# Kernel tuning notes

Hardware: AMD Instinct MI355X
Metric: run time of the kernel (lower is better)

Reference implementation:

```python
import jax, jax.numpy as jnp
import numpy as np

EPS = 1e-5

def _bn(x, s, o):
    m = jnp.mean(x, axis=(0, 1), keepdims=True)
    v = jnp.var(x, axis=(0, 1), keepdims=True)
    return (x - m) * jax.lax.rsqrt(v + EPS) * s + o

def _conv1d(x, w):
    return jax.lax.conv_general_dilated(x, w, (1,), 'SAME', dimension_numbers=('NWC', 'WIO', 'NWC'))

def _lstm_step(x, h, c, W, b):
    g = jnp.concatenate([x, h], -1) @ W + b
    i, gg, f, o = jnp.split(g, 4, -1)
    c = jax.nn.sigmoid(f + 1.0) * c + jax.nn.sigmoid(i) * jnp.tanh(gg)
    h = jax.nn.sigmoid(o) * jnp.tanh(c)
    return h, c

def setup_inputs() -> dict:
    key = jax.random.key(0)
    ks = jax.random.split(key, 24)
    B, L, T = 16, 256, 512
    V, E, H, MEL, P = 256, 256, 512, 80, 512
    f = lambda k, shape, s: jax.random.normal(k, shape, jnp.float32) * s
    inp = {}
    inp['phonemes'] = jax.random.randint(ks[0], (B, L), 0, V, dtype=jnp.int32)
    inp['lengths'] = jnp.full((B,), L, dtype=jnp.int32)
    inp['mels'] = jax.random.normal(ks[1], (B, T, MEL), jnp.float32)
    inp['durations'] = jax.random.uniform(ks[2], (B, L), jnp.float32, 1.0, 3.0)
    for i, n in enumerate(['zm_h1', 'zm_c1', 'zm_h2', 'zm_c2']):
        inp[n] = jax.random.bernoulli(ks[3 + i], 0.1, (B, T, H))
    inp['embed'] = f(ks[7], (V, E), 1.0)
    inp['enc_conv_w'] = f(ks[8], (3, 3, E, E), 0.05)
    inp['enc_bn_s'] = jnp.ones((3, E)); inp['enc_bn_o'] = jnp.zeros((3, E))
    inp['lstm_fwd_w'] = f(ks[9], (2 * E, 4 * E), 0.05); inp['lstm_fwd_b'] = jnp.zeros((4 * E,))
    inp['lstm_bwd_w'] = f(ks[10], (2 * E, 4 * E), 0.05); inp['lstm_bwd_b'] = jnp.zeros((4 * E,))
    inp['prenet_w1'] = f(ks[11], (MEL, 256), 0.05); inp['prenet_bn1_s'] = jnp.ones((256,)); inp['prenet_bn1_o'] = jnp.zeros((256,))
    inp['prenet_w2'] = f(ks[12], (256, 256), 0.05); inp['prenet_bn2_s'] = jnp.ones((256,)); inp['prenet_bn2_o'] = jnp.zeros((256,))
    D_in = 2 * E + 256  # cond(512)+prenet(256)=768
    inp['dec_w1'] = f(ks[13], (D_in + H, 4 * H), 0.03); inp['dec_b1'] = jnp.zeros((4 * H,))
    inp['dec_w2'] = f(ks[14], (D_in + H + H, 4 * H), 0.03); inp['dec_b2'] = jnp.zeros((4 * H,))
    inp['proj_w'] = f(ks[15], (2 * E + 2 * H, MEL), 0.03); inp['proj_b'] = jnp.zeros((MEL,))
    inp['post_w0'] = f(ks[16], (5, MEL, P), 0.05)
    inp['post_w_mid'] = f(ks[17], (3, 5, P, P), 0.03)
    inp['post_w4'] = f(ks[18], (5, P, MEL), 0.03); inp['post_b4'] = jnp.zeros((MEL,))
    inp['post_bn_s'] = jnp.ones((4, P)); inp['post_bn_o'] = jnp.zeros((4, P))
    return inp

def reference(phonemes, lengths, mels, durations, zm_h1, zm_c1, zm_h2, zm_c2,
              embed, enc_conv_w, enc_bn_s, enc_bn_o,
              lstm_fwd_w, lstm_fwd_b, lstm_bwd_w, lstm_bwd_b,
              prenet_w1, prenet_bn1_s, prenet_bn1_o, prenet_w2, prenet_bn2_s, prenet_bn2_o,
              dec_w1, dec_b1, dec_w2, dec_b2, proj_w, proj_b,
              post_w0, post_w_mid, post_w4, post_b4, post_bn_s, post_bn_o):
    x = embed[phonemes]                                   # [B,L,E]
    for i in range(3):
        x = jax.nn.relu(_bn(_conv1d(x, enc_conv_w[i]), enc_bn_s[i], enc_bn_o[i]))
    B, L, E = x.shape
    mask = jnp.arange(L)[None, :] >= (lengths[:, None] - 1)  # [B,L] reset signal for bwd core
    x_t = jnp.swapaxes(x, 0, 1)                           # [L,B,E] time-major
    h0 = jnp.zeros((B, E), x.dtype)

    def fwd_step(carry, xt):
        h, c = carry
        h, c = _lstm_step(xt, h, c, lstm_fwd_w, lstm_fwd_b)
        return (h, c), h
    _, h_fwd = jax.lax.scan(fwd_step, (h0, h0), x_t)

    x_b = jnp.flip(x_t, axis=0)
    r_b = jnp.flip(jnp.swapaxes(mask, 0, 1), axis=0)      # [L,B]

    def bwd_step(carry, inp):
        xt, rt = inp
        h, c = carry
        h = jnp.where(rt[:, None], 0.0, h)  # ResetCore: reset state to initial where flagged
        c = jnp.where(rt[:, None], 0.0, c)
        h, c = _lstm_step(xt, h, c, lstm_bwd_w, lstm_bwd_b)
        return (h, c), h
    _, h_bwd = jax.lax.scan(bwd_step, (h0, h0), (x_b, r_b))
    enc = jnp.swapaxes(jnp.concatenate([h_fwd, jnp.flip(h_bwd, axis=0)], -1), 0, 1)  # [B,L,2E]

    # ---- duration-based Gaussian-softmax upsampling ----
    T = mels.shape[1]
    ruler = jnp.arange(T, dtype=durations.dtype)[None, :]
    mid_pos = jnp.cumsum(durations, axis=1) - durations / 2  # [B,L]
    d2 = jnp.square(mid_pos[:, None, :] - ruler[:, :, None]) / 10.0  # [B,T,L]
    w = jax.nn.softmax(-d2, axis=-1)
    cond = jnp.einsum('btl,bld->btd', w, enc)             # [B,T,512]

    # ---- prenet on teacher-forced mels ----
    p = jax.nn.relu(_bn(mels @ prenet_w1, prenet_bn1_s, prenet_bn1_o))
    p = jax.nn.relu(_bn(p @ prenet_w2, prenet_bn2_s, prenet_bn2_o))
    dec_in = jnp.concatenate([cond, p], axis=-1)          # [B,T,768]

    # ---- 2-layer skip-connection LSTM decoder with zoneout ----
    H = dec_w1.shape[1] // 4
    s0 = jnp.zeros((B, H), dec_in.dtype)
    xs = (jnp.swapaxes(dec_in, 0, 1),
          jnp.swapaxes(zm_h1, 0, 1), jnp.swapaxes(zm_c1, 0, 1),
          jnp.swapaxes(zm_h2, 0, 1), jnp.swapaxes(zm_c2, 0, 1))

    def dec_step(carry, inp):
        h1, c1, h2, c2 = carry
        xt, mh1, mc1, mh2, mc2 = inp
        nh1, nc1 = _lstm_step(xt, h1, c1, dec_w1, dec_b1)
        in2 = jnp.concatenate([xt, nh1], -1)              # skip connection
        nh2, nc2 = _lstm_step(in2, h2, c2, dec_w2, dec_b2)
        out = jnp.concatenate([nh1, nh2], -1)
        zo = lambda m, so, sn: jnp.where(m, so, sn)       # zoneout: keep old state w.p. 0.1
        return (zo(mh1, h1, nh1), zo(mc1, c1, nc1), zo(mh2, h2, nh2), zo(mc2, c2, nc2)), out
    _, dec_out = jax.lax.scan(dec_step, (s0, s0, s0, s0), xs)
    dec_out = jnp.swapaxes(dec_out, 0, 1)                 # [B,T,2H]

    mel_pred = jnp.concatenate([cond, dec_out], -1) @ proj_w + proj_b  # [B,T,80]

    y = jnp.tanh(_bn(_conv1d(mel_pred, post_w0), post_bn_s[0], post_bn_o[0]))
    for i in range(3):
        y = jnp.tanh(_bn(_conv1d(y, post_w_mid[i]), post_bn_s[i + 1], post_bn_o[i + 1]))
    residual = _conv1d(y, post_w4) + post_b4
    return (mel_pred, mel_pred + residual)
```

## Files before the change

### kernel.cpp

```cpp
#include <hip/hip_runtime.h>

#define EPSV 1e-5f

typedef unsigned int uivec4 __attribute__((ext_vector_type(4)));
typedef short bh8 __attribute__((ext_vector_type(8)));
typedef float f32x4 __attribute__((ext_vector_type(4)));

__device__ __forceinline__ float b2f(unsigned short u) {
  unsigned int x = ((unsigned int)u) << 16;
  return __uint_as_float(x);
}
__device__ __forceinline__ unsigned short f2b(float f) {
  unsigned int x = __float_as_uint(f);
  unsigned int r = (x + 0x7FFFu + ((x >> 16) & 1u)) >> 16;
  return (unsigned short)r;
}
__device__ __forceinline__ float sigm(float x) { return 1.0f / (1.0f + expf(-x)); }

__device__ __forceinline__ void stg_bf16(unsigned short* p, float v) {
  unsigned short h = f2b(v);
  asm volatile("global_store_short %0, %1, off sc0 sc1" ::"v"(p), "v"(h) : "memory");
}
__device__ __forceinline__ void ldg2_sc(const unsigned short* p0, const unsigned short* p1,
                                        uivec4& a, uivec4& b) {
  asm volatile(
      "global_load_dwordx4 %0, %2, off sc0 sc1\n\t"
      "global_load_dwordx4 %1, %3, off sc0 sc1\n\t"
      "s_waitcnt vmcnt(0)"
      : "=&v"(a), "=&v"(b)
      : "v"(p0), "v"(p1)
      : "memory");
}
__device__ __forceinline__ void ldg4f_nw(const unsigned short* p, uivec4& a, uivec4& b,
                                         uivec4& c, uivec4& d) {
  asm volatile(
      "global_load_dwordx4 %0, %4, off sc0 sc1\n\t"
      "global_load_dwordx4 %1, %4, off offset:256 sc0 sc1\n\t"
      "global_load_dwordx4 %2, %4, off offset:512 sc0 sc1\n\t"
      "global_load_dwordx4 %3, %4, off offset:768 sc0 sc1"
      : "=&v"(a), "=&v"(b), "=&v"(c), "=&v"(d)
      : "v"(p)
      : "memory");
}
__device__ __forceinline__ void vm0() { asm volatile("s_waitcnt vmcnt(0)" ::: "memory"); }
__device__ __forceinline__ unsigned int ldcnt(const unsigned int* p) {
  return __hip_atomic_load(p, __ATOMIC_RELAXED, __HIP_MEMORY_SCOPE_AGENT);
}

__global__ void k_detect(const void* __restrict__ embp, const void* __restrict__ zmp,
                         int* __restrict__ flags) {
  __shared__ int sh[4];
  int tid = threadIdx.x;
  if (tid < 4) sh[tid] = 0;
  __syncthreads();
  const unsigned short* u = (const unsigned short*)embp;
  int bad = 0;
  for (int i = tid; i < 4096; i += 256) {
    float f = fabsf(b2f(u[i]));
    if (!(f < 1e10f)) bad = 1;
  }
  if (bad) atomicAdd(&sh[3], 1);
  const unsigned char* p = (const unsigned char*)zmp;
  int codd = 0, c0 = 0, c1v = 0;
  for (int i = tid; i < 65536; i += 256) {
    unsigned char v = p[i];
    if (v) {
      if (i & 1) codd++;
      if ((i & 3) == 0) c0++;
      if (v == 1) c1v++;
    }
  }
  atomicAdd(&sh[0], codd); atomicAdd(&sh[1], c0); atomicAdd(&sh[2], c1v);
  __syncthreads();
  if (tid == 0) {
    flags[0] = sh[3] ? 1 : 0;
    int mode;
    if (sh[0] == 0) mode = 1;
    else if (sh[2] > 0) mode = 0;
    else if (sh[1] == 0) mode = 2;
    else mode = 3;
    flags[1] = mode;
  }
}

__global__ void k_cvt(const void* __restrict__ src, float* __restrict__ dst, int n,
                      const int* __restrict__ flags) {
  int i = blockIdx.x * 256 + threadIdx.x;
  if (i >= n) return;
  if (flags[0]) dst[i] = ((const float*)src)[i];
  else dst[i] = b2f(((const unsigned short*)src)[i]);
}

__global__ void k_cvtb(const float* __restrict__ src, unsigned short* __restrict__ dst, int n) {
  int i = blockIdx.x * 256 + threadIdx.x;
  if (i >= n) return;
  dst[i] = f2b(src[i]);
}

__global__ void k_cvtbp(const float* __restrict__ src, unsigned short* __restrict__ dst,
                        int K, int Kpad) {
  int r = blockIdx.x;
  int c = threadIdx.x;
  if (c < Kpad)
    dst[(size_t)r * Kpad + c] = (c < K) ? f2b(src[(size_t)r * K + c]) : (unsigned short)0;
}

__device__ __forceinline__ bool mask_at(const void* p, size_t i, int mode) {
  switch (mode) {
    case 0: return ((const unsigned char*)p)[i] != 0;
    case 1: return ((const int*)p)[i] != 0;
    case 2: return ((const float*)p)[i] != 0.0f;
    default: return ((const unsigned short*)p)[i] != 0;
  }
}

__global__ void k_embed(const int* __restrict__ ph, const float* __restrict__ emb,
                        float* __restrict__ X) {
  int bl = blockIdx.x;
  int p = ph[bl];
  X[(size_t)bl * 256 + threadIdx.x] = emb[(size_t)p * 256 + threadIdx.x];
}

__global__ __launch_bounds__(256) void k_cs1(const float* __restrict__ X, int RB, int C,
                                             float* __restrict__ part) {
  int blk = blockIdx.x;
  int r0 = blk * RB;
  float s0 = 0.f, q0 = 0.f, s1 = 0.f, q1 = 0.f;
  for (int rr = 0; rr < RB; ++rr) {
    const float* row = X + (size_t)(r0 + rr) * C;
    float v = row[threadIdx.x];
    s0 += v; q0 += v * v;
    if (C > 256) {
      float v1 = row[256 + threadIdx.x];
      s1 += v1; q1 += v1 * v1;
    }
  }
  float* pr = part + (size_t)blk * 2 * C;
  pr[threadIdx.x] = s0;
  pr[C + threadIdx.x] = q0;
  if (C > 256) {
    pr[256 + threadIdx.x] = s1;
    pr[C + 256 + threadIdx.x] = q1;
  }
}
__global__ __launch_bounds__(256) void k_cs2(const float* __restrict__ part, int C, int R,
                                             float* __restrict__ st) {
  int c = blockIdx.x;
  int t = threadIdx.x;
  __shared__ float rs_[256], rq_[256];
  rs_[t] = part[(size_t)t * 2 * C + c];
  rq_[t] = part[(size_t)t * 2 * C + C + c];
  __syncthreads();
  for (int k = 128; k > 0; k >>= 1) {
    if (t < k) { rs_[t] += rs_[t + k]; rq_[t] += rq_[t + k]; }
    __syncthreads();
  }
  if (t == 0) {
    float m = rs_[0] / R;
    st[c] = m;
    st[C + c] = rq_[0] / R - m * m;
  }
}

template <int ACT>
__global__ void k_bnact(const float* __restrict__ X, float* __restrict__ Y,
                        const float* __restrict__ st, const float* __restrict__ sc,
                        const float* __restrict__ of, int Cmask, int n) {
  int i = blockIdx.x * 256 + threadIdx.x;
  if (i >= n) return;
  int C = Cmask + 1;
  int c = i & Cmask;
  float m = st[c], v = st[C + c];
  float y = (X[i] - m) * rsqrtf(v + EPSV) * sc[c] + of[c];
  Y[i] = ACT ? tanhf(y) : fmaxf(y, 0.0f);
}

__global__ __launch_bounds__(256) void k_trbp(const float* __restrict__ src, int ldn,
                                              unsigned short* __restrict__ dst,
                                              int K, int Kpad, int N, int Npad) {
  __shared__ float tl[64][65];
  int k0 = blockIdx.x * 64, n0 = blockIdx.y * 64;
  int tid = threadIdx.x;
#pragma unroll
  for (int p = 0; p < 16; ++p) {
    int idx = p * 256 + tid;
    int r = idx >> 6, c = idx & 63;
    float v = 0.0f;
    if (k0 + r < K && n0 + c < N) v = src[(size_t)(k0 + r) * ldn + n0 + c];
    tl[r][c] = v;
  }
  __syncthreads();
#pragma unroll
  for (int p = 0; p < 16; ++p) {
    int idx = p * 256 + tid;
    int rr = idx >> 6, cc = idx & 63;
    if (n0 + rr < Npad && k0 + cc < Kpad)
      dst[(size_t)(n0 + rr) * Kpad + k0 + cc] = f2b(tl[cc][rr]);
  }
}

__global__ __launch_bounds__(256) void k_i2c3(const float* __restrict__ X,
                                              unsigned short* __restrict__ out) {
  int r = blockIdx.x;
  int b = r >> 8, l = r & 255;
#pragma unroll
  for (int p = 0; p < 3; ++p) {
    int col = p * 256 + threadIdx.x;
    int d = col >> 8, ci = col & 255;
    int ll = l + d - 1;
    float v = (ll >= 0 && ll < 256) ? X[(size_t)(b * 256 + ll) * 256 + ci] : 0.0f;
    out[(size_t)r * 768 + col] = f2b(v);
  }
}
__global__ __launch_bounds__(256) void k_i2c(const float* __restrict__ X,
                                             unsigned short* __restrict__ out) {
  int r = blockIdx.x;
  int b = r >> 9, t = r & 511;
#pragma unroll
  for (int p = 0; p < 10; ++p) {
    int col = p * 256 + threadIdx.x;
    int dt = col >> 9, ci = col & 511;
    int tt = t + dt - 2;
    float v = (tt >= 0 && tt < 512) ? X[((size_t)(b * 512 + tt)) * 512 + ci] : 0.0f;
    out[(size_t)r * 2560 + col] = f2b(v);
  }
}
__global__ __launch_bounds__(256) void k_i2c80(const float* __restrict__ X,
                                               unsigned short* __restrict__ out) {
  int r = blockIdx.x;
  int b = r >> 9, t = r & 511;
#pragma unroll
  for (int p = 0; p < 2; ++p) {
    int col = p * 256 + threadIdx.x;
    if (col < 416) {
      float v = 0.0f;
      if (col < 400) {
        int dt = col / 80, ci = col - dt * 80;
        int tt = t + dt - 2;
        if (tt >= 0 && tt < 512) v = X[(size_t)(b * 512 + tt) * 80 + ci];
      }
      out[(size_t)r * 416 + col] = f2b(v);
    }
  }
}

__global__ __launch_bounds__(256) void k_cat3b(const float* __restrict__ cond,
                                               const float* __restrict__ h1n,
                                               const float* __restrict__ h2n,
                                               unsigned short* __restrict__ out) {
  int r = blockIdx.x;
  int b = r >> 9, t = r & 511;
#pragma unroll
  for (int p = 0; p < 6; ++p) {
    int col = p * 256 + threadIdx.x;
    float v;
    if (col < 512) v = cond[(size_t)r * 512 + col];
    else if (col < 1024) v = h1n[(size_t)(t * 16 + b) * 512 + (col - 512)];
    else v = h2n[(size_t)(t * 16 + b) * 512 + (col - 1024)];
    out[(size_t)r * 1536 + col] = f2b(v);
  }
}

template <int OBF>
__global__ __launch_bounds__(256) void k_mf(const unsigned short* __restrict__ A,
                                            const unsigned short* __restrict__ Bt,
                                            const float* __restrict__ bias,
                                            void* __restrict__ Cp, int M, int N, int K,
                                            int Nst) {
  const int lane = threadIdx.x & 63, wv = threadIdx.x >> 6;
  const int m0 = blockIdx.x * 64 + wv * 16;
  const int n0 = blockIdx.y * 64;
  const int koff = (lane >> 4) << 3;
  const unsigned short* arow = A + (size_t)(m0 + (lane & 15)) * K + koff;
  const unsigned short* brow0 = Bt + (size_t)(n0 + 0 * 16 + (lane & 15)) * K + koff;
  const unsigned short* brow1 = Bt + (size_t)(n0 + 1 * 16 + (lane & 15)) * K + koff;
  const unsigned short* brow2 = Bt + (size_t)(n0 + 2 * 16 + (lane & 15)) * K + koff;
  const unsigned short* brow3 = Bt + (size_t)(n0 + 3 * 16 + (lane & 15)) * K + koff;
  f32x4 acc0 = {0.f, 0.f, 0.f, 0.f}, acc1 = {0.f, 0.f, 0.f, 0.f};
  f32x4 acc2 = {0.f, 0.f, 0.f, 0.f}, acc3 = {0.f, 0.f, 0.f, 0.f};
  for (int k = 0; k < K; k += 32) {
    bh8 a = *(const bh8*)(arow + k);
    bh8 b0 = *(const bh8*)(brow0 + k);
    bh8 b1 = *(const bh8*)(brow1 + k);
    bh8 b2 = *(const bh8*)(brow2 + k);
    bh8 b3 = *(const bh8*)(brow3 + k);
    acc0 = __builtin_amdgcn_mfma_f32_16x16x32_bf16(a, b0, acc0, 0, 0, 0);
    acc1 = __builtin_amdgcn_mfma_f32_16x16x32_bf16(a, b1, acc1, 0, 0, 0);
    acc2 = __builtin_amdgcn_mfma_f32_16x16x32_bf16(a, b2, acc2, 0, 0, 0);
    acc3 = __builtin_amdgcn_mfma_f32_16x16x32_bf16(a, b3, acc3, 0, 0, 0);
  }
  const int r0 = m0 + ((lane >> 4) << 2);
  const int nl = lane & 15;
  float av[4][4];
#pragma unroll
  for (int r = 0; r < 4; ++r) { av[0][r] = acc0[r]; av[1][r] = acc1[r]; av[2][r] = acc2[r]; av[3][r] = acc3[r]; }
#pragma unroll
  for (int t = 0; t < 4; ++t) {
    int n = n0 + t * 16 + nl;
    float bv = 0.0f;
    if (bias) {
      if (OBF == 4) bv = (n < Nst) ? bias[n] : 0.0f;
      else bv = bias[n];
    }
#pragma unroll
    for (int r = 0; r < 4; ++r) {
      float v = av[t][r] + bv;
      int row = r0 + r;
      if (OBF == 0) {
        ((float*)Cp)[(size_t)row * N + n] = v;
      } else if (OBF == 4) {
        if (n < Nst) ((float*)Cp)[(size_t)row * Nst + n] = v;
      } else if (OBF == 2) {
        int b = row >> 9, tt = row & 511;
        int g = n >> 9, w = (n & 511) >> 2, jj = n & 3;
        ((unsigned short*)Cp)[((size_t)tt * 128 + w) * 256 + b * 16 + g * 4 + jj] = f2b(v);
      } else {
        int b = row >> 8, l = row & 255;
        int g = n >> 8, w = (n & 255) >> 2, jj = n & 3;
        ((float*)Cp)[((size_t)l * 64 + w) * 256 + b * 16 + g * 4 + jj] = v;
      }
    }
  }
}

__global__ void k_cumsum(const float* __restrict__ dur, float* __restrict__ mid) {
  int b = threadIdx.x;
  if (b >= 16) return;
  float run = 0.f;
  for (int l = 0; l < 256; ++l) {
    float d = dur[b * 256 + l];
    run += d;
    mid[b * 256 + l] = run - 0.5f * d;
  }
}

#define EST 130
__global__ __launch_bounds__(256) void k_enc_lstm(const float* __restrict__ GFp,
                                                  const float* __restrict__ GBp,
                                                  const float* __restrict__ Wf,
                                                  const float* __restrict__ Wb,
                                                  float* __restrict__ enc,
                                                  unsigned short* __restrict__ encB,
                                                  const int* __restrict__ lengths,
                                                  unsigned int* __restrict__ cnt) {
  const int tid = threadIdx.x;
  const int wg = blockIdx.x;
  const int dir = wg >> 6;
  const int w = wg & 63;
  const float* Gpre = dir ? GBp : GFp;
  const float* W = dir ? Wb : Wf;
  unsigned int* c_self = cnt + (size_t)dir * 256 * 128;

  __shared__ __align__(16) unsigned int hsW[16 * EST];
  __shared__ __align__(16) float accb[4 * 264];
  __shared__ __align__(16) float gl[256];
  __shared__ float cst[64];
  __shared__ int rs[16];

  const int lane = tid & 63, wv = tid >> 6;
  const int n16 = lane & 15, lq = lane >> 4;
  const int colg = (n16 & 3) * 256 + w * 4 + (n16 >> 2);
  bh8 BE[2];
#pragma unroll
  for (int c = 0; c < 2; ++c) {
#pragma unroll
    for (int jj = 0; jj < 8; ++jj) {
      int k = (wv * 2 + c) * 32 + lq * 8 + jj;
      BE[c][jj] = (short)f2b(W[(size_t)(256 + k) * 1024 + colg]);
    }
  }
  if (tid < 64) cst[tid] = 0.0f;
  __syncthreads();

  const int b_ = tid >> 4, j_ = (tid >> 2) & 3, g_ = tid & 3;

  for (int t = 0; t < 256; ++t) {
    const int l = dir ? (255 - t) : t;
    if (tid < 16) rs[tid] = (dir == 1) && (l >= lengths[tid] - 1);
    float gpre = Gpre[((size_t)l * 64 + w) * 256 + b_ * 16 + g_ * 4 + j_];
    if (t > 0 && tid < 8) {
      const unsigned int* a = c_self + (size_t)(t - 1) * 128 + tid * 16;
      unsigned int gcount = 0;
      while (ldcnt(a) < 8u) {
        __builtin_amdgcn_s_sleep(2);
        if (++gcount > (1u << 16)) break;
      }
    }
    __syncthreads();
    if (t > 0) {
      const int lprev = dir ? (l + 1) : (l - 1);
      int b = tid >> 4, q = tid & 15;
      const unsigned short* p = encB + ((size_t)dir << 20) + (((size_t)lprev * 16 + b) << 8) + q * 16;
      uivec4 a0, a1;
      ldg2_sc(p, p + 8, a0, a1);
      if (rs[b]) {
        a0.x = a0.y = a0.z = a0.w = 0u;
        a1.x = a1.y = a1.z = a1.w = 0u;
      }
      *(uivec4*)&hsW[b * EST + q * 8] = a0;
      *(uivec4*)&hsW[b * EST + q * 8 + 4] = a1;
    }
    __syncthreads();

    f32x4 acc = {0.f, 0.f, 0.f, 0.f};
    if (t > 0) {
#pragma unroll
      for (int c = 0; c < 2; ++c) {
        int kw = (wv * 2 + c) * 16 + lq * 4;
        bh8 af = *(const bh8*)&hsW[(lane & 15) * EST + kw];
        acc = __builtin_amdgcn_mfma_f32_16x16x32_bf16(af, BE[c], acc, 0, 0, 0);
      }
    }
    {
      int idx = lq * 64 + (lane & 15);
      float* pb = &accb[wv * 264];
#pragma unroll
      for (int r = 0; r < 4; ++r) pb[idx + r * 16] = acc[r];
    }
    __syncthreads();
    gl[tid] = gpre + accb[tid] + accb[264 + tid] + accb[528 + tid] + accb[792 + tid];
    __syncthreads();
    if (tid < 64) {
      int b = tid >> 2, j = tid & 3;
      float4 G = ((const float4*)gl)[tid];
      float c = cst[tid];
      if (t == 0 || rs[b]) c = 0.0f;
      c = sigm(G.z + 1.0f) * c + sigm(G.x) * tanhf(G.y);
      float h = sigm(G.w) * tanhf(c);
      cst[tid] = c;
      enc[(size_t)(b * 256 + l) * 512 + dir * 256 + (w * 4 + j)] = h;
      stg_bf16(&encB[((size_t)dir << 20) + (((size_t)l * 16 + b) << 8) + (w * 4 + j)], h);
    }
    vm0();
    __syncthreads();
    if (tid == 0)
      __hip_atomic_fetch_add(c_self + (size_t)t * 128 + (w >> 3) * 16, 1u,
                             __ATOMIC_RELAXED, __HIP_MEMORY_SCOPE_AGENT);
  }
}

__global__ __launch_bounds__(256) void k_upsample(const float* __restrict__ mid,
                                                  const float* __restrict__ enc,
                                                  float* __restrict__ cond) {
  int blk = blockIdx.x;
  int b = blk >> 5, t0 = (blk & 31) * 16;
  int tid = threadIdx.x;
  __shared__ float wls[16][256];
  __shared__ float red[256];
  float mp = mid[b * 256 + tid];
  for (int tt = 0; tt < 16; ++tt) {
    float tpos = (float)(t0 + tt);
    float d = mp - tpos;
    float d2 = d * d * 0.1f;
    red[tid] = d2; __syncthreads();
    for (int k = 128; k > 0; k >>= 1) { if (tid < k) red[tid] = fminf(red[tid], red[tid + k]); __syncthreads(); }
    float mn = red[0]; __syncthreads();
    float e = expf(mn - d2);
    red[tid] = e; __syncthreads();
    for (int k = 128; k > 0; k >>= 1) { if (tid < k) red[tid] += red[tid + k]; __syncthreads(); }
    float sum = red[0]; __syncthreads();
    wls[tt][tid] = e / sum;
  }
  __syncthreads();
  float a0[16], a1[16];
#pragma unroll
  for (int i = 0; i < 16; ++i) { a0[i] = 0; a1[i] = 0; }
  for (int l = 0; l < 256; ++l) {
    float e0 = enc[(size_t)(b * 256 + l) * 512 + tid];
    float e1 = enc[(size_t)(b * 256 + l) * 512 + 256 + tid];
#pragma unroll
    for (int tt = 0; tt < 16; ++tt) { float wv = wls[tt][l]; a0[tt] += wv * e0; a1[tt] += wv * e1; }
  }
  for (int tt = 0; tt < 16; ++tt) {
    cond[(size_t)(b * 512 + t0 + tt) * 512 + tid] = a0[tt];
    cond[(size_t)(b * 512 + t0 + tt) * 512 + 256 + tid] = a1[tt];
  }
}

__global__ void k_concat(const float* __restrict__ cond, const float* __restrict__ p,
                         unsigned short* __restrict__ din) {
  size_t i = (size_t)blockIdx.x * 256 + threadIdx.x;
  int r = (int)(i / 768);
  int c = (int)(i % 768);
  float v = (c < 512) ? cond[(size_t)r * 512 + c] : p[(size_t)r * 256 + (c - 512)];
  din[i] = f2b(v);
}

#define DST 780
__global__ __launch_bounds__(256) void k_dec_lstm(
    const unsigned short* __restrict__ D1x, const unsigned short* __restrict__ D2x,
    const float* __restrict__ W1, const float* __restrict__ W2,
    const void* __restrict__ zh1, const void* __restrict__ zc1,
    const void* __restrict__ zh2, const void* __restrict__ zc2,
    unsigned short* __restrict__ h1cB, unsigned short* __restrict__ h1nB,
    unsigned short* __restrict__ h2cB,
    float* __restrict__ h1n, float* __restrict__ h2n,
    unsigned int* __restrict__ cnt1,
    const int* __restrict__ flags) {
  const int tid = threadIdx.x;
  const int w = blockIdx.x;

  __shared__ __align__(16) unsigned int hsW[16 * DST];
  __shared__ __align__(16) float accb[8 * 264];
  __shared__ __align__(16) float gl1[256], gl2[256];
  __shared__ float cst1[64], hst1[64], cst2[64], hst2[64];

  const int mmode = flags[1];
  const int lane = tid & 63, wv = tid >> 6;
  const int n16 = lane & 15, lq = lane >> 4;
  const int colg = (n16 & 3) * 512 + w * 4 + (n16 >> 2);

  bh8 B1[4], B2[8];
#pragma unroll
  for (int c = 0; c < 4; ++c) {
#pragma unroll
    for (int jj = 0; jj < 8; ++jj) {
      int k = (wv * 4 + c) * 32 + lq * 8 + jj;
      B1[c][jj] = (short)f2b(W1[(size_t)(768 + k) * 2048 + colg]);
    }
  }
#pragma unroll
  for (int c = 0; c < 8; ++c) {
#pragma unroll
    for (int jj = 0; jj < 8; ++jj) {
      int k = (wv * 8 + c) * 32 + lq * 8 + jj;
      B2[c][jj] = (short)f2b(W2[(size_t)(768 + k) * 2048 + colg]);
    }
  }
  if (tid < 64) { cst1[tid] = 0; hst1[tid] = 0; cst2[tid] = 0; hst2[tid] = 0; }
  __syncthreads();

  const int b_ = tid >> 4, j_ = (tid >> 2) & 3, g_ = tid & 3;

  for (int tau = 0; tau <= 512; ++tau) {
    float dxv1 = 0.0f, dxv2 = 0.0f;
    if (tau < 512)
      dxv1 = b2f(D1x[((size_t)tau * 128 + w) * 256 + b_ * 16 + g_ * 4 + j_]);
    if (tau >= 1)
      dxv2 = b2f(D2x[((size_t)(tau - 1) * 128 + w) * 256 + b_ * 16 + g_ * 4 + j_]);

    if (tau >= 1 && tid < 8) {
      const unsigned int* a = cnt1 + (size_t)(tau - 1) * 128 + tid * 16;
      unsigned int gcount = 0;
      while (ldcnt(a) < 16u) {
        __builtin_amdgcn_s_sleep(2);
        if (++gcount > (1u << 16)) break;
      }
    }
    __syncthreads();

    if (tau >= 1) {
      int b = tid >> 4, q = tid & 15;
      const unsigned short* p0 = h1cB + (((size_t)(tau - 1) * 16 + b) << 9) + q * 8;
      const unsigned short* p1 = h1nB + (((size_t)(tau - 1) * 16 + b) << 9) + q * 8;
      uivec4 r[12];
      ldg4f_nw(p0, r[0], r[1], r[2], r[3]);
      ldg4f_nw(p1, r[4], r[5], r[6], r[7]);
      if (tau >= 2) {
        const unsigned short* p2 = h2cB + (((size_t)(tau - 2) * 16 + b) << 9) + q * 8;
        ldg4f_nw(p2, r[8], r[9], r[10], r[11]);
      } else {
        uivec4 z; z.x = z.y = z.z = z.w = 0u;
        r[8] = z; r[9] = z; r[10] = z; r[11] = z;
      }
      vm0();
      unsigned int base = b * DST + q * 4;
#pragma unroll
      for (int m = 0; m < 4; ++m) *(uivec4*)&hsW[base + 64 * m] = r[m];
#pragma unroll
      for (int m = 0; m < 4; ++m) *(uivec4*)&hsW[base + 256 + 64 * m] = r[4 + m];
#pragma unroll
      for (int m = 0; m < 4; ++m) *(uivec4*)&hsW[base + 512 + 64 * m] = r[8 + m];
    }
    __syncthreads();

    f32x4 a1 = {0.f, 0.f, 0.f, 0.f}, a2 = {0.f, 0.f, 0.f, 0.f};
    if (tau >= 1) {
      if (tau < 512) {
#pragma unroll
        for (int c = 0; c < 4; ++c) {
          int kw = (wv * 4 + c) * 16 + lq * 4;
          bh8 af = *(const bh8*)&hsW[(lane & 15) * DST + kw];
          a1 = __builtin_amdgcn_mfma_f32_16x16x32_bf16(af, B1[c], a1, 0, 0, 0);
        }
      }
#pragma unroll
      for (int c = 0; c < 8; ++c) {
        int kw = 256 + (wv * 8 + c) * 16 + lq * 4;
        bh8 af = *(const bh8*)&hsW[(lane & 15) * DST + kw];
        a2 = __builtin_amdgcn_mfma_f32_16x16x32_bf16(af, B2[c], a2, 0, 0, 0);
      }
    }
    {
      int idx = lq * 64 + (lane & 15);
      float* p1b = &accb[wv * 264];
      float* p2b = &accb[(4 + wv) * 264];
#pragma unroll
      for (int r = 0; r < 4; ++r) p1b[idx + r * 16] = a1[r];
#pragma unroll
      for (int r = 0; r < 4; ++r) p2b[idx + r * 16] = a2[r];
    }
    __syncthreads();
    gl1[tid] = dxv1 + accb[tid] + accb[264 + tid] + accb[528 + tid] + accb[792 + tid];
    gl2[tid] = dxv2 + accb[1056 + tid] + accb[1320 + tid] + accb[1584 + tid] + accb[1848 + tid];
    __syncthreads();

    if (tid < 64) {
      if (tau < 512) {
        int b = tid >> 2, j = tid & 3, colgw = w * 4 + j;
        float4 G = ((const float4*)gl1)[tid];
        float cold = (tau == 0) ? 0.0f : cst1[tid];
        float hold = (tau == 0) ? 0.0f : hst1[tid];
        float nc = sigm(G.z + 1.0f) * cold + sigm(G.x) * tanhf(G.y);
        float nh = sigm(G.w) * tanhf(nc);
        size_t mi = ((size_t)b * 512 + tau) * 512 + colgw;
        bool mh = mask_at(zh1, mi, mmode);
        bool mc = mask_at(zc1, mi, mmode);
        cst1[tid] = mc ? cold : nc;
        float hkeep = mh ? hold : nh;
        hst1[tid] = hkeep;
        h1n[(size_t)(tau * 16 + b) * 512 + colgw] = nh;
        stg_bf16(&h1cB[(((size_t)tau * 16 + b) << 9) + colgw], hkeep);
        stg_bf16(&h1nB[(((size_t)tau * 16 + b) << 9) + colgw], nh);
      }
    } else if (tid < 128) {
      if (tau >= 1) {
        int u = tid - 64;
        int t2 = tau - 1;
        int b = u >> 2, j = u & 3, colgw = w * 4 + j;
        float4 G = ((const float4*)gl2)[u];
        float cold = (tau == 1) ? 0.0f : cst2[u];
        float hold = (tau == 1) ? 0.0f : hst2[u];
        float nc = sigm(G.z + 1.0f) * cold + sigm(G.x) * tanhf(G.y);
        float nh = sigm(G.w) * tanhf(nc);
        size_t mi = ((size_t)b * 512 + t2) * 512 + colgw;
        bool mh = mask_at(zh2, mi, mmode);
        bool mc = mask_at(zc2, mi, mmode);
        cst2[u] = mc ? cold : nc;
        float hkeep = mh ? hold : nh;
        hst2[u] = hkeep;
        h2n[(size_t)(t2 * 16 + b) * 512 + colgw] = nh;
        stg_bf16(&h2cB[(((size_t)t2 * 16 + b) << 9) + colgw], hkeep);
      }
    }
    vm0();
    __syncthreads();
    if (tid == 0)
      __hip_atomic_fetch_add(cnt1 + (size_t)tau * 128 + (w >> 4) * 16, 1u,
                             __ATOMIC_RELAXED, __HIP_MEMORY_SCOPE_AGENT);
  }
}

__global__ void k_out(const float* __restrict__ mel, const float* __restrict__ res,
                      void* __restrict__ out, const int* __restrict__ flags) {
  int i = blockIdx.x * 256 + threadIdx.x;
  float m = mel[i];
  float f = m + res[i];
  if (flags[0]) {
    ((float*)out)[i] = m;
    ((float*)out)[655360 + i] = f;
  } else {
    unsigned short* o = (unsigned short*)out;
    o[i] = f2b(m);
    o[655360 + i] = f2b(f);
  }
}

extern "C" void kernel_launch(void* const* d_in, const int* in_sizes, int n_in,
                              void* d_out, int out_size, void* d_ws, size_t ws_size,
                              hipStream_t stream) {
  char* ws = (char*)d_ws;
  size_t o = 0;
  auto A_ = [&](size_t nb) { size_t r = o; o += (nb + 255) & ~(size_t)255; return r; };
  const size_t FLAGS = A_(256);
  const size_t SYNC = A_(786432);
  const size_t STATS = A_(4096);
  const size_t PARTS = A_(1048576 + 4096);
  const size_t XAB = A_(2097152);
  const size_t WTE1 = A_(524288), WTE2 = A_(524288);
  const size_t C_MELS = A_(655360ull * 4), C_DUR = A_(4096 * 4), C_EMB = A_(65536 * 4),
               C_ECW = A_(589824ull * 4), C_EBS = A_(768 * 4), C_EBO = A_(768 * 4),
               C_LFW = A_(524288ull * 4), C_LFB = A_(1024 * 4), C_LBW = A_(524288ull * 4),
               C_LBB = A_(1024 * 4), C_PW1 = A_(20480 * 4), C_P1S = A_(256 * 4),
               C_P1O = A_(256 * 4), C_PW2 = A_(65536 * 4), C_P2S = A_(256 * 4),
               C_P2O = A_(256 * 4), C_DW1 = A_(2621440ull * 4), C_DB1 = A_(2048 * 4),
               C_DW2 = A_(3670016ull * 4), C_DB2 = A_(2048 * 4), C_PRW = A_(122880ull * 4),
               C_PRB = A_(512), C_W0 = A_(204800ull * 4), C_WM = A_(3932160ull * 4),
               C_W4 = A_(204800ull * 4), C_B4 = A_(512), C_PBS = A_(2048 * 4),
               C_PBO = A_(2048 * 4);
  const size_t R1 = A_(16777216), R2 = A_(16777216), R3 = A_(16777216), R4 = A_(16777216),
               MID = A_(4096 * 4), R5 = A_(16777216), R6 = A_(16777216), R7 = A_(25165824),
               D1X = A_(33554432), D2X = A_(33554432), MELP = A_(2621440);
  const size_t XA = R1, XB = R1 + 4194304;
  const size_t XCOL3 = R2, ECWT = R3;
  const size_t GF = R2;
  const size_t GB = R3, H1N = R3;
  const size_t ENC = R4, H2N = R4;
  const size_t COND = R5, PA = R5;
  const size_t PREA = R6, PREB = R6 + 8388608, PB = R6;
  const size_t DECIN = R7, RESID = R7;
  const size_t H1CB = R1, H1NB = R1 + 8388608;
  const size_t H2CB = R2;
  const size_t ENCB = R7;
  const size_t MELB = R1, PW1T = R1 + 2097152, PREBB = R1, PW2T = R1 + 8388608;
  const size_t WT1 = R4, WT2 = R4 + 4194304;
  const size_t PROJA = R1;
  const size_t PRWT = R6;
  const size_t XCOL80 = R1, W0T = R2;
  const size_t XCOL = R1;
  const size_t WTP = D1X, W4T = D2X;

  auto F = [&](size_t off) { return (float*)(ws + off); };
  auto U = [&](size_t off) { return (unsigned short*)(ws + off); };
  int* flags = (int*)(ws + FLAGS);
  unsigned int* cntE = (unsigned int*)(ws + SYNC);
  unsigned int* cnt1 = (unsigned int*)(ws + SYNC + 262144);

  hipMemsetAsync(ws + SYNC, 0, 786432, stream);
  k_detect<<<1, 256, 0, stream>>>(d_in[8], d_in[4], flags);

  struct CV { int idx; size_t off; int n; };
  const CV cvs[] = {
      {2, C_MELS, 655360}, {3, C_DUR, 4096}, {8, C_EMB, 65536}, {9, C_ECW, 589824},
      {10, C_EBS, 768}, {11, C_EBO, 768}, {12, C_LFW, 524288}, {13, C_LFB, 1024},
      {14, C_LBW, 524288}, {15, C_LBB, 1024}, {16, C_PW1, 20480}, {17, C_P1S, 256},
      {18, C_P1O, 256}, {19, C_PW2, 65536}, {20, C_P2S, 256}, {21, C_P2O, 256},
      {22, C_DW1, 2621440}, {23, C_DB1, 2048}, {24, C_DW2, 3670016}, {25, C_DB2, 2048},
      {26, C_PRW, 122880}, {27, C_PRB, 80}, {28, C_W0, 204800}, {29, C_WM, 3932160},
      {30, C_W4, 204800}, {31, C_B4, 80}, {32, C_PBS, 2048}, {33, C_PBO, 2048}};
  for (int i = 0; i < (int)(sizeof(cvs) / sizeof(cvs[0])); ++i)
    k_cvt<<<(cvs[i].n + 255) / 256, 256, 0, stream>>>(d_in[cvs[i].idx], F(cvs[i].off), cvs[i].n, flags);

  k_embed<<<4096, 256, 0, stream>>>((const int*)d_in[0], F(C_EMB), F(XA));
  for (int i = 0; i < 3; ++i) {
    k_i2c3<<<4096, 256, 0, stream>>>(F(XA), U(XCOL3));
    k_trbp<<<dim3(12, 4), 256, 0, stream>>>(F(C_ECW) + (size_t)i * 196608, 256, U(ECWT), 768, 768, 256, 256);
    k_mf<0><<<dim3(64, 4), 256, 0, stream>>>(U(XCOL3), U(ECWT), nullptr, (void*)(ws + XB), 4096, 256, 768, 256);
    k_cs1<<<256, 256, 0, stream>>>(F(XB), 16, 256, F(PARTS));
    k_cs2<<<256, 256, 0, stream>>>(F(PARTS), 256, 4096, F(STATS));
    k_bnact<0><<<4096, 256, 0, stream>>>(F(XB), F(XA), F(STATS), F(C_EBS) + i * 256, F(C_EBO) + i * 256, 255, 1048576);
  }
  k_cvtb<<<4096, 256, 0, stream>>>(F(XA), U(XAB), 1048576);
  k_trbp<<<dim3(4, 16), 256, 0, stream>>>(F(C_LFW), 1024, U(WTE1), 256, 256, 1024, 1024);
  k_trbp<<<dim3(4, 16), 256, 0, stream>>>(F(C_LBW), 1024, U(WTE2), 256, 256, 1024, 1024);
  k_mf<3><<<dim3(64, 16), 256, 0, stream>>>(U(XAB), U(WTE1), F(C_LFB), (void*)(ws + GF), 4096, 1024, 256, 1024);
  k_mf<3><<<dim3(64, 16), 256, 0, stream>>>(U(XAB), U(WTE2), F(C_LBB), (void*)(ws + GB), 4096, 1024, 256, 1024);
  k_cumsum<<<1, 64, 0, stream>>>(F(C_DUR), F(MID));
  k_enc_lstm<<<128, 256, 0, stream>>>(F(GF), F(GB), F(C_LFW), F(C_LBW), F(ENC), U(ENCB),
                                      (const int*)d_in[1], cntE);
  k_upsample<<<512, 256, 0, stream>>>(F(MID), F(ENC), F(COND));

  k_cvtbp<<<8192, 128, 0, stream>>>(F(C_MELS), U(MELB), 80, 96);
  k_trbp<<<dim3(2, 4), 256, 0, stream>>>(F(C_PW1), 256, U(PW1T), 80, 96, 256, 256);
  k_mf<0><<<dim3(128, 4), 256, 0, stream>>>(U(MELB), U(PW1T), nullptr, (void*)(ws + PREA), 8192, 256, 96, 256);
  k_cs1<<<256, 256, 0, stream>>>(F(PREA), 32, 256, F(PARTS));
  k_cs2<<<256, 256, 0, stream>>>(F(PARTS), 256, 8192, F(STATS));
  k_bnact<0><<<8192, 256, 0, stream>>>(F(PREA), F(PREB), F(STATS), F(C_P1S), F(C_P1O), 255, 2097152);
  k_cvtb<<<8192, 256, 0, stream>>>(F(PREB), U(PREBB), 2097152);
  k_trbp<<<dim3(4, 4), 256, 0, stream>>>(F(C_PW2), 256, U(PW2T), 256, 256, 256, 256);
  k_mf<0><<<dim3(128, 4), 256, 0, stream>>>(U(PREBB), U(PW2T), nullptr, (void*)(ws + PREA), 8192, 256, 256, 256);
  k_cs1<<<256, 256, 0, stream>>>(F(PREA), 32, 256, F(PARTS));
  k_cs2<<<256, 256, 0, stream>>>(F(PARTS), 256, 8192, F(STATS));
  k_bnact<0><<<8192, 256, 0, stream>>>(F(PREA), F(PREB), F(STATS), F(C_P2S), F(C_P2O), 255, 2097152);

  k_concat<<<24576, 256, 0, stream>>>(F(COND), F(PREB), U(DECIN));
  k_trbp<<<dim3(12, 32), 256, 0, stream>>>(F(C_DW1), 2048, U(WT1), 768, 768, 2048, 2048);
  k_trbp<<<dim3(12, 32), 256, 0, stream>>>(F(C_DW2), 2048, U(WT2), 768, 768, 2048, 2048);
  k_mf<2><<<dim3(128, 32), 256, 0, stream>>>(U(DECIN), U(WT1), F(C_DB1), (void*)(ws + D1X), 8192, 2048, 768, 2048);
  k_mf<2><<<dim3(128, 32), 256, 0, stream>>>(U(DECIN), U(WT2), F(C_DB2), (void*)(ws + D2X), 8192, 2048, 768, 2048);
  k_dec_lstm<<<128, 256, 0, stream>>>((const unsigned short*)(ws + D1X), (const unsigned short*)(ws + D2X),
                                      F(C_DW1), F(C_DW2), d_in[4], d_in[5], d_in[6], d_in[7],
                                      U(H1CB), U(H1NB), U(H2CB),
                                      F(H1N), F(H2N), cnt1, flags);
  k_cat3b<<<8192, 256, 0, stream>>>(F(COND), F(H1N), F(H2N), U(PROJA));
  k_trbp<<<dim3(24, 2), 256, 0, stream>>>(F(C_PRW), 80, U(PRWT), 1536, 1536, 80, 128);
  k_mf<4><<<dim3(128, 2), 256, 0, stream>>>(U(PROJA), U(PRWT), F(C_PRB), (void*)(ws + MELP), 8192, 128, 1536, 80);

  k_i2c80<<<8192, 256, 0, stream>>>(F(MELP), U(XCOL80));
  k_trbp<<<dim3(7, 8), 256, 0, stream>>>(F(C_W0), 512, U(W0T), 400, 416, 512, 512);
  k_mf<0><<<dim3(128, 8), 256, 0, stream>>>(U(XCOL80), U(W0T), nullptr, (void*)(ws + PA), 8192, 512, 416, 512);
  k_cs1<<<256, 256, 0, stream>>>(F(PA), 32, 512, F(PARTS));
  k_cs2<<<512, 256, 0, stream>>>(F(PARTS), 512, 8192, F(STATS));
  k_bnact<1><<<16384, 256, 0, stream>>>(F(PA), F(PB), F(STATS), F(C_PBS), F(C_PBO), 511, 4194304);
  for (int i = 0; i < 3; ++i) {
    k_i2c<<<8192, 256, 0, stream>>>(F(PB), U(XCOL));
    k_trbp<<<dim3(40, 8), 256, 0, stream>>>(F(C_WM) + (size_t)i * 1310720, 512, U(WTP), 2560, 2560, 512, 512);
    k_mf<0><<<dim3(128, 8), 256, 0, stream>>>(U(XCOL), U(WTP), nullptr, (void*)(ws + PA), 8192, 512, 2560, 512);
    k_cs1<<<256, 256, 0, stream>>>(F(PA), 32, 512, F(PARTS));
    k_cs2<<<512, 256, 0, stream>>>(F(PARTS), 512, 8192, F(STATS));
    k_bnact<1><<<16384, 256, 0, stream>>>(F(PA), F(PB), F(STATS), F(C_PBS) + (i + 1) * 512, F(C_PBO) + (i + 1) * 512, 511, 4194304);
  }
  k_i2c<<<8192, 256, 0, stream>>>(F(PB), U(XCOL));
  k_trbp<<<dim3(40, 2), 256, 0, stream>>>(F(C_W4), 80, U(W4T), 2560, 2560, 80, 128);
  k_mf<4><<<dim3(128, 2), 256, 0, stream>>>(U(XCOL), U(W4T), F(C_B4), (void*)(ws + RESID), 8192, 128, 2560, 80);
  k_out<<<2560, 256, 0, stream>>>(F(MELP), F(RESID), d_out, flags);
}
```

Baseline: 5.237 ms.

## Fuse im2col into conv GEMMs and halve workgroups in recurrent LSTM kernels

The conv layers now use a new implicit-im2col MFMA GEMM kernel (k_mfc) that reads the bf16 activations directly. This removes the separate im2col kernels and their large intermediate buffers. The BN/activation and embedding kernels also write a bf16 copy, so a separate conversion pass is no longer needed. Separately, the encoder and decoder LSTM kernels are remapped so each workgroup handles 8 hidden units instead of 4 (64 workgroups instead of 128), which reduces cross-workgroup barrier participants per step at the cost of more MFMA and work per block.

Measured after the change: 4.875 ms (median of 2 runs). -6.9%, faster.

```diff
diff --git a/kernel.cpp b/kernel.cpp
--- a/kernel.cpp
+++ b/kernel.cpp
@@ -115,10 +115,12 @@
 }
 
 __global__ void k_embed(const int* __restrict__ ph, const float* __restrict__ emb,
-                        float* __restrict__ X) {
+                        float* __restrict__ X, unsigned short* __restrict__ Xb) {
   int bl = blockIdx.x;
   int p = ph[bl];
-  X[(size_t)bl * 256 + threadIdx.x] = emb[(size_t)p * 256 + threadIdx.x];
+  float v = emb[(size_t)p * 256 + threadIdx.x];
+  X[(size_t)bl * 256 + threadIdx.x] = v;
+  Xb[(size_t)bl * 256 + threadIdx.x] = f2b(v);
 }
 
 __global__ __launch_bounds__(256) void k_cs1(const float* __restrict__ X, int RB, int C,
@@ -164,6 +166,7 @@
 
 template <int ACT>
 __global__ void k_bnact(const float* __restrict__ X, float* __restrict__ Y,
+                        unsigned short* __restrict__ Yb,
                         const float* __restrict__ st, const float* __restrict__ sc,
                         const float* __restrict__ of, int Cmask, int n) {
   int i = blockIdx.x * 256 + threadIdx.x;
@@ -172,7 +175,9 @@
   int c = i & Cmask;
   float m = st[c], v = st[C + c];
   float y = (X[i] - m) * rsqrtf(v + EPSV) * sc[c] + of[c];
-  Y[i] = ACT ? tanhf(y) : fmaxf(y, 0.0f);
+  float r = ACT ? tanhf(y) : fmaxf(y, 0.0f);
+  Y[i] = r;
+  if (Yb) Yb[i] = f2b(r);
 }
 
 __global__ __launch_bounds__(256) void k_trbp(const float* __restrict__ src, int ldn,
@@ -196,51 +201,6 @@
     int rr = idx >> 6, cc = idx & 63;
     if (n0 + rr < Npad && k0 + cc < Kpad)
       dst[(size_t)(n0 + rr) * Kpad + k0 + cc] = f2b(tl[cc][rr]);
-  }
-}
-
-__global__ __launch_bounds__(256) void k_i2c3(const float* __restrict__ X,
-                                              unsigned short* __restrict__ out) {
-  int r = blockIdx.x;
-  int b = r >> 8, l = r & 255;
-#pragma unroll
-  for (int p = 0; p < 3; ++p) {
-    int col = p * 256 + threadIdx.x;
-    int d = col >> 8, ci = col & 255;
-    int ll = l + d - 1;
-    float v = (ll >= 0 && ll < 256) ? X[(size_t)(b * 256 + ll) * 256 + ci] : 0.0f;
-    out[(size_t)r * 768 + col] = f2b(v);
-  }
-}
-__global__ __launch_bounds__(256) void k_i2c(const float* __restrict__ X,
-                                             unsigned short* __restrict__ out) {
-  int r = blockIdx.x;
-  int b = r >> 9, t = r & 511;
-#pragma unroll
-  for (int p = 0; p < 10; ++p) {
-    int col = p * 256 + threadIdx.x;
-    int dt = col >> 9, ci = col & 511;
-    int tt = t + dt - 2;
-    float v = (tt >= 0 && tt < 512) ? X[((size_t)(b * 512 + tt)) * 512 + ci] : 0.0f;
-    out[(size_t)r * 2560 + col] = f2b(v);
-  }
-}
-__global__ __launch_bounds__(256) void k_i2c80(const float* __restrict__ X,
-                                               unsigned short* __restrict__ out) {
-  int r = blockIdx.x;
-  int b = r >> 9, t = r & 511;
-#pragma unroll
-  for (int p = 0; p < 2; ++p) {
-    int col = p * 256 + threadIdx.x;
-    if (col < 416) {
-      float v = 0.0f;
-      if (col < 400) {
-        int dt = col / 80, ci = col - dt * 80;
-        int tt = t + dt - 2;
-        if (tt >= 0 && tt < 512) v = X[(size_t)(b * 512 + tt) * 80 + ci];
-      }
-      out[(size_t)r * 416 + col] = f2b(v);
-    }
   }
 }
 
@@ -323,6 +283,67 @@
   }
 }
 
+template <int KW, int CIN, int TT, int OBF>
+__global__ __launch_bounds__(256) void k_mfc(const unsigned short* __restrict__ Xb,
+                                             const unsigned short* __restrict__ Bt,
+                                             const float* __restrict__ bias,
+                                             void* __restrict__ Cp, int M, int N, int K,
+                                             int Nst) {
+  const int lane = threadIdx.x & 63, wv = threadIdx.x >> 6;
+  const int m0 = blockIdx.x * 64 + wv * 16;
+  const int n0 = blockIdx.y * 64;
+  const int koff = (lane >> 4) << 3;
+  const int row = m0 + (lane & 15);
+  const int bb = row / TT, t = row % TT;
+  const unsigned short* brow0 = Bt + (size_t)(n0 + 0 * 16 + (lane & 15)) * K + koff;
+  const unsigned short* brow1 = Bt + (size_t)(n0 + 1 * 16 + (lane & 15)) * K + koff;
+  const unsigned short* brow2 = Bt + (size_t)(n0 + 2 * 16 + (lane & 15)) * K + koff;
+  const unsigned short* brow3 = Bt + (size_t)(n0 + 3 * 16 + (lane & 15)) * K + koff;
+  f32x4 acc0 = {0.f, 0.f, 0.f, 0.f}, acc1 = {0.f, 0.f, 0.f, 0.f};
+  f32x4 acc2 = {0.f, 0.f, 0.f, 0.f}, acc3 = {0.f, 0.f, 0.f, 0.f};
+  for (int k = 0; k < K; k += 32) {
+    int ke = k + koff;
+    int dt = ke / CIN;
+    int ci = ke - dt * CIN;
+    int tt = t + dt - (KW / 2);
+    bh8 a = {0, 0, 0, 0, 0, 0, 0, 0};
+    if (dt < KW && tt >= 0 && tt < TT)
+      a = *(const bh8*)&Xb[((size_t)(bb * TT + tt)) * CIN + ci];
+    bh8 b0 = *(const bh8*)(brow0 + k);
+    bh8 b1 = *(const bh8*)(brow1 + k);
+    bh8 b2 = *(const bh8*)(brow2 + k);
+    bh8 b3 = *(const bh8*)(brow3 + k);
+    acc0 = __builtin_amdgcn_mfma_f32_16x16x32_bf16(a, b0, acc0, 0, 0, 0);
+    acc1 = __builtin_amdgcn_mfma_f32_16x16x32_bf16(a, b1, acc1, 0, 0, 0);
+    acc2 = __builtin_amdgcn_mfma_f32_16x16x32_bf16(a, b2, acc2, 0, 0, 0);
+    acc3 = __builtin_amdgcn_mfma_f32_16x16x32_bf16(a, b3, acc3, 0, 0, 0);
+  }
+  const int r0 = m0 + ((lane >> 4) << 2);
+  const int nl = lane & 15;
+  float av[4][4];
+#pragma unroll
+  for (int r = 0; r < 4; ++r) { av[0][r] = acc0[r]; av[1][r] = acc1[r]; av[2][r] = acc2[r]; av[3][r] = acc3[r]; }
+#pragma unroll
+  for (int tq = 0; tq < 4; ++tq) {
+    int n = n0 + tq * 16 + nl;
+    float bv = 0.0f;
+    if (bias) {
+      if (OBF == 4) bv = (n < Nst) ? bias[n] : 0.0f;
+      else bv = bias[n];
+    }
+#pragma unroll
+    for (int r = 0; r < 4; ++r) {
+      float v = av[tq][r] + bv;
+      int rw = r0 + r;
+      if (OBF == 0) {
+        ((float*)Cp)[(size_t)rw * N + n] = v;
+      } else if (OBF == 4) {
+        if (n < Nst) ((float*)Cp)[(size_t)rw * Nst + n] = v;
+      }
+    }
+  }
+}
+
 __global__ void k_cumsum(const float* __restrict__ dur, float* __restrict__ mid) {
   int b = threadIdx.x;
   if (b >= 16) return;
@@ -345,43 +366,53 @@
                                                   unsigned int* __restrict__ cnt) {
   const int tid = threadIdx.x;
   const int wg = blockIdx.x;
-  const int dir = wg >> 6;
-  const int w = wg & 63;
+  const int dir = wg >> 5;
+  const int w = wg & 31;
   const float* Gpre = dir ? GBp : GFp;
   const float* W = dir ? Wb : Wf;
   unsigned int* c_self = cnt + (size_t)dir * 256 * 128;
 
   __shared__ __align__(16) unsigned int hsW[16 * EST];
-  __shared__ __align__(16) float accb[4 * 264];
-  __shared__ __align__(16) float gl[256];
-  __shared__ float cst[64];
+  __shared__ __align__(16) float accb[8 * 264];
+  __shared__ __align__(16) float gl[16 * 33];
+  __shared__ float cst[128];
   __shared__ int rs[16];
 
   const int lane = tid & 63, wv = tid >> 6;
   const int n16 = lane & 15, lq = lane >> 4;
-  const int colg = (n16 & 3) * 256 + w * 4 + (n16 >> 2);
-  bh8 BE[2];
-#pragma unroll
-  for (int c = 0; c < 2; ++c) {
-#pragma unroll
-    for (int jj = 0; jj < 8; ++jj) {
-      int k = (wv * 2 + c) * 32 + lq * 8 + jj;
-      BE[c][jj] = (short)f2b(W[(size_t)(256 + k) * 1024 + colg]);
-    }
-  }
-  if (tid < 64) cst[tid] = 0.0f;
+
+  bh8 BE[2][2];
+#pragma unroll
+  for (int s = 0; s < 2; ++s) {
+    int n = s * 16 + n16;
+    int colg = (n >> 3) * 256 + w * 8 + (n & 7);
+#pragma unroll
+    for (int c = 0; c < 2; ++c)
+#pragma unroll
+      for (int j = 0; j < 8; ++j) {
+        int k = wv * 64 + c * 32 + lq * 8 + j;
+        BE[c][s][j] = (short)f2b(W[(size_t)(256 + k) * 1024 + colg]);
+      }
+  }
+  if (tid < 128) cst[tid] = 0.0f;
   __syncthreads();
-
-  const int b_ = tid >> 4, j_ = (tid >> 2) & 3, g_ = tid & 3;
 
   for (int t = 0; t < 256; ++t) {
     const int l = dir ? (255 - t) : t;
     if (tid < 16) rs[tid] = (dir == 1) && (l >= lengths[tid] - 1);
-    float gpre = Gpre[((size_t)l * 64 + w) * 256 + b_ * 16 + g_ * 4 + j_];
+    float gp[2];
+#pragma unroll
+    for (int it = 0; it < 2; ++it) {
+      int e = tid + it * 256;
+      int b = e >> 5, n = e & 31;
+      int jn = n & 7, g = n >> 3;
+      int slot = w * 2 + (jn >> 2);
+      gp[it] = Gpre[((size_t)l * 64 + slot) * 256 + b * 16 + g * 4 + (jn & 3)];
+    }
     if (t > 0 && tid < 8) {
       const unsigned int* a = c_self + (size_t)(t - 1) * 128 + tid * 16;
       unsigned int gcount = 0;
-      while (ldcnt(a) < 8u) {
+      while (ldcnt(a) < 4u) {
         __builtin_amdgcn_s_sleep(2);
         if (++gcount > (1u << 16)) break;
       }
@@ -402,39 +433,58 @@
     }
     __syncthreads();
 
-    f32x4 acc = {0.f, 0.f, 0.f, 0.f};
+    f32x4 ac[2] = {{0.f, 0.f, 0.f, 0.f}, {0.f, 0.f, 0.f, 0.f}};
     if (t > 0) {
 #pragma unroll
       for (int c = 0; c < 2; ++c) {
-        int kw = (wv * 2 + c) * 16 + lq * 4;
+        int kw = wv * 32 + c * 16 + lq * 4;
         bh8 af = *(const bh8*)&hsW[(lane & 15) * EST + kw];
-        acc = __builtin_amdgcn_mfma_f32_16x16x32_bf16(af, BE[c], acc, 0, 0, 0);
+        ac[0] = __builtin_amdgcn_mfma_f32_16x16x32_bf16(af, BE[c][0], ac[0], 0, 0, 0);
+        ac[1] = __builtin_amdgcn_mfma_f32_16x16x32_bf16(af, BE[c][1], ac[1], 0, 0, 0);
       }
     }
     {
-      int idx = lq * 64 + (lane & 15);
-      float* pb = &accb[wv * 264];
-#pragma unroll
-      for (int r = 0; r < 4; ++r) pb[idx + r * 16] = acc[r];
-    }
-    __syncthreads();
-    gl[tid] = gpre + accb[tid] + accb[264 + tid] + accb[528 + tid] + accb[792 + tid];
-    __syncthreads();
-    if (tid < 64) {
-      int b = tid >> 2, j = tid & 3;
-      float4 G = ((const float4*)gl)[tid];
+      int idx = (lq * 4) * 16 + n16;
+#pragma unroll
+      for (int s = 0; s < 2; ++s) {
+        float* pb = &accb[(s * 4 + wv) * 264];
+#pragma unroll
+        for (int r = 0; r < 4; ++r) pb[idx + r * 16] = ac[s][r];
+      }
+    }
+    __syncthreads();
+#pragma unroll
+    for (int it = 0; it < 2; ++it) {
+      int e = tid + it * 256;
+      int b = e >> 5, n = e & 31;
+      int s = n >> 4, nn = n & 15;
+      float sum = gp[it];
+      if (t > 0) {
+#pragma unroll
+        for (int v = 0; v < 4; ++v) sum += accb[(s * 4 + v) * 264 + b * 16 + nn];
+      }
+      gl[b * 33 + n] = sum;
+    }
+    __syncthreads();
+    if (tid < 128) {
+      int b = tid >> 3, jn = tid & 7;
+      float gi = gl[b * 33 + 0 * 8 + jn];
+      float gg = gl[b * 33 + 1 * 8 + jn];
+      float gf = gl[b * 33 + 2 * 8 + jn];
+      float go = gl[b * 33 + 3 * 8 + jn];
       float c = cst[tid];
       if (t == 0 || rs[b]) c = 0.0f;
-      c = sigm(G.z + 1.0f) * c + sigm(G.x) * tanhf(G.y);
-      float h = sigm(G.w) * tanhf(c);
+      c = sigm(gf + 1.0f) * c + sigm(gi) * tanhf(gg);
+      float h = sigm(go) * tanhf(c);
       cst[tid] = c;
-      enc[(size_t)(b * 256 + l) * 512 + dir * 256 + (w * 4 + j)] = h;
-      stg_bf16(&encB[((size_t)dir << 20) + (((size_t)l * 16 + b) << 8) + (w * 4 + j)], h);
+      int col = w * 8 + jn;
+      enc[(size_t)(b * 256 + l) * 512 + dir * 256 + col] = h;
+      stg_bf16(&encB[((size_t)dir << 20) + (((size_t)l * 16 + b) << 8) + col], h);
     }
     vm0();
     __syncthreads();
     if (tid == 0)
-      __hip_atomic_fetch_add(c_self + (size_t)t * 128 + (w >> 3) * 16, 1u,
+      __hip_atomic_fetch_add(c_self + (size_t)t * 128 + (w >> 2) * 16, 1u,
                              __ATOMIC_RELAXED, __HIP_MEMORY_SCOPE_AGENT);
   }
 }
@@ -501,48 +551,64 @@
   const int w = blockIdx.x;
 
   __shared__ __align__(16) unsigned int hsW[16 * DST];
-  __shared__ __align__(16) float accb[8 * 264];
-  __shared__ __align__(16) float gl1[256], gl2[256];
-  __shared__ float cst1[64], hst1[64], cst2[64], hst2[64];
+  __shared__ __align__(16) float accb1[8 * 264];
+  __shared__ __align__(16) float accb2[8 * 264];
+  __shared__ __align__(16) float gl1[16 * 33], gl2[16 * 33];
+  __shared__ float cst1[128], hst1[128], cst2[128], hst2[128];
 
   const int mmode = flags[1];
   const int lane = tid & 63, wv = tid >> 6;
   const int n16 = lane & 15, lq = lane >> 4;
-  const int colg = (n16 & 3) * 512 + w * 4 + (n16 >> 2);
-
-  bh8 B1[4], B2[8];
-#pragma unroll
-  for (int c = 0; c < 4; ++c) {
-#pragma unroll
-    for (int jj = 0; jj < 8; ++jj) {
-      int k = (wv * 4 + c) * 32 + lq * 8 + jj;
-      B1[c][jj] = (short)f2b(W1[(size_t)(768 + k) * 2048 + colg]);
-    }
-  }
-#pragma unroll
-  for (int c = 0; c < 8; ++c) {
-#pragma unroll
-    for (int jj = 0; jj < 8; ++jj) {
-      int k = (wv * 8 + c) * 32 + lq * 8 + jj;
-      B2[c][jj] = (short)f2b(W2[(size_t)(768 + k) * 2048 + colg]);
-    }
-  }
-  if (tid < 64) { cst1[tid] = 0; hst1[tid] = 0; cst2[tid] = 0; hst2[tid] = 0; }
+
+  bh8 B1[4][2], B2[8][2];
+#pragma unroll
+  for (int s = 0; s < 2; ++s) {
+    int n = s * 16 + n16;
+    int colg = (n >> 3) * 512 + w * 8 + (n & 7);
+#pragma unroll
+    for (int c = 0; c < 4; ++c)
+#pragma unroll
+      for (int j = 0; j < 8; ++j) {
+        int k = wv * 128 + c * 32 + lq * 8 + j;
+        B1[c][s][j] = (short)f2b(W1[(size_t)(768 + k) * 2048 + colg]);
+      }
+#pragma unroll
+    for (int c = 0; c < 8; ++c)
+#pragma unroll
+      for (int j = 0; j < 8; ++j) {
+        int k = wv * 256 + c * 32 + lq * 8 + j;
+        B2[c][s][j] = (short)f2b(W2[(size_t)(768 + k) * 2048 + colg]);
+      }
+  }
+  if (tid < 128) { cst1[tid] = 0; hst1[tid] = 0; cst2[tid] = 0; hst2[tid] = 0; }
   __syncthreads();
 
-  const int b_ = tid >> 4, j_ = (tid >> 2) & 3, g_ = tid & 3;
-
   for (int tau = 0; tau <= 512; ++tau) {
-    float dxv1 = 0.0f, dxv2 = 0.0f;
-    if (tau < 512)
-      dxv1 = b2f(D1x[((size_t)tau * 128 + w) * 256 + b_ * 16 + g_ * 4 + j_]);
-    if (tau >= 1)
-      dxv2 = b2f(D2x[((size_t)(tau - 1) * 128 + w) * 256 + b_ * 16 + g_ * 4 + j_]);
-
+    float dx1[2] = {0.f, 0.f}, dx2[2] = {0.f, 0.f};
+    if (tau < 512) {
+#pragma unroll
+      for (int it = 0; it < 2; ++it) {
+        int e = tid + it * 256;
+        int b = e >> 5, n = e & 31;
+        int jn = n & 7, g = n >> 3;
+        int slot = w * 2 + (jn >> 2);
+        dx1[it] = b2f(D1x[((size_t)tau * 128 + slot) * 256 + b * 16 + g * 4 + (jn & 3)]);
+      }
+    }
+    if (tau >= 1) {
+#pragma unroll
+      for (int it = 0; it < 2; ++it) {
+        int e = tid + it * 256;
+        int b = e >> 5, n = e & 31;
+        int jn = n & 7, g = n >> 3;
+        int slot = w * 2 + (jn >> 2);
+        dx2[it] = b2f(D2x[((size_t)(tau - 1) * 128 + slot) * 256 + b * 16 + g * 4 + (jn & 3)]);
+      }
+    }
     if (tau >= 1 && tid < 8) {
       const unsigned int* a = cnt1 + (size_t)(tau - 1) * 128 + tid * 16;
       unsigned int gcount = 0;
-      while (ldcnt(a) < 16u) {
+      while (ldcnt(a) < 8u) {
         __builtin_amdgcn_s_sleep(2);
         if (++gcount > (1u << 16)) break;
       }
@@ -574,45 +640,68 @@
     }
     __syncthreads();
 
-    f32x4 a1 = {0.f, 0.f, 0.f, 0.f}, a2 = {0.f, 0.f, 0.f, 0.f};
+    f32x4 a1[2] = {{0.f, 0.f, 0.f, 0.f}, {0.f, 0.f, 0.f, 0.f}};
+    f32x4 a2[2] = {{0.f, 0.f, 0.f, 0.f}, {0.f, 0.f, 0.f, 0.f}};
     if (tau >= 1) {
       if (tau < 512) {
 #pragma unroll
         for (int c = 0; c < 4; ++c) {
-          int kw = (wv * 4 + c) * 16 + lq * 4;
+          int kw = wv * 64 + c * 16 + lq * 4;
           bh8 af = *(const bh8*)&hsW[(lane & 15) * DST + kw];
-          a1 = __builtin_amdgcn_mfma_f32_16x16x32_bf16(af, B1[c], a1, 0, 0, 0);
+          a1[0] = __builtin_amdgcn_mfma_f32_16x16x32_bf16(af, B1[c][0], a1[0], 0, 0, 0);
+          a1[1] = __builtin_amdgcn_mfma_f32_16x16x32_bf16(af, B1[c][1], a1[1], 0, 0, 0);
         }
       }
 #pragma unroll
       for (int c = 0; c < 8; ++c) {
-        int kw = 256 + (wv * 8 + c) * 16 + lq * 4;
+        int kw = 256 + wv * 128 + c * 16 + lq * 4;
         bh8 af = *(const bh8*)&hsW[(lane & 15) * DST + kw];
-        a2 = __builtin_amdgcn_mfma_f32_16x16x32_bf16(af, B2[c], a2, 0, 0, 0);
+        a2[0] = __builtin_amdgcn_mfma_f32_16x16x32_bf16(af, B2[c][0], a2[0], 0, 0, 0);
+        a2[1] = __builtin_amdgcn_mfma_f32_16x16x32_bf16(af, B2[c][1], a2[1], 0, 0, 0);
       }
     }
     {
-      int idx = lq * 64 + (lane & 15);
-      float* p1b = &accb[wv * 264];
-      float* p2b = &accb[(4 + wv) * 264];
-#pragma unroll
-      for (int r = 0; r < 4; ++r) p1b[idx + r * 16] = a1[r];
-#pragma unroll
-      for (int r = 0; r < 4; ++r) p2b[idx + r * 16] = a2[r];
-    }
-    __syncthreads();
-    gl1[tid] = dxv1 + accb[tid] + accb[264 + tid] + accb[528 + tid] + accb[792 + tid];
-    gl2[tid] = dxv2 + accb[1056 + tid] + accb[1320 + tid] + accb[1584 + tid] + accb[1848 + tid];
-    __syncthreads();
-
-    if (tid < 64) {
+      int idx = (lq * 4) * 16 + n16;
+#pragma unroll
+      for (int s = 0; s < 2; ++s) {
+        float* p1b = &accb1[(s * 4 + wv) * 264];
+        float* p2b = &accb2[(s * 4 + wv) * 264];
+#pragma unroll
+        for (int r = 0; r < 4; ++r) { p1b[idx + r * 16] = a1[s][r]; p2b[idx + r * 16] = a2[s][r]; }
+      }
+    }
+    __syncthreads();
+#pragma unroll
+    for (int it = 0; it < 2; ++it) {
+      int e = tid + it * 256;
+      int b = e >> 5, n = e & 31;
+      int s = n >> 4, nn = n & 15;
+      int off = b * 16 + nn;
+      float s1 = dx1[it], s2 = dx2[it];
+      if (tau >= 1) {
+        if (tau < 512) {
+#pragma unroll
+          for (int v = 0; v < 4; ++v) s1 += accb1[(s * 4 + v) * 264 + off];
+        }
+#pragma unroll
+        for (int v = 0; v < 4; ++v) s2 += accb2[(s * 4 + v) * 264 + off];
+      }
+      gl1[b * 33 + n] = s1;
+      gl2[b * 33 + n] = s2;
+    }
+    __syncthreads();
+
+    if (tid < 128) {
       if (tau < 512) {
-        int b = tid >> 2, j = tid & 3, colgw = w * 4 + j;
-        float4 G = ((const float4*)gl1)[tid];
+        int b = tid >> 3, jn = tid & 7, colgw = w * 8 + jn;
+        float gi = gl1[b * 33 + 0 * 8 + jn];
+        float gg = gl1[b * 33 + 1 * 8 + jn];
+        float gf = gl1[b * 33 + 2 * 8 + jn];
+        float go = gl1[b * 33 + 3 * 8 + jn];
         float cold = (tau == 0) ? 0.0f : cst1[tid];
         float hold = (tau == 0) ? 0.0f : hst1[tid];
-        float nc = sigm(G.z + 1.0f) * cold + sigm(G.x) * tanhf(G.y);
-        float nh = sigm(G.w) * tanhf(nc);
+        float nc = sigm(gf + 1.0f) * cold + sigm(gi) * tanhf(gg);
+        float nh = sigm(go) * tanhf(nc);
         size_t mi = ((size_t)b * 512 + tau) * 512 + colgw;
         bool mh = mask_at(zh1, mi, mmode);
         bool mc = mask_at(zc1, mi, mmode);
@@ -623,16 +712,19 @@
         stg_bf16(&h1cB[(((size_t)tau * 16 + b) << 9) + colgw], hkeep);
         stg_bf16(&h1nB[(((size_t)tau * 16 + b) << 9) + colgw], nh);
       }
-    } else if (tid < 128) {
+    } else {
       if (tau >= 1) {
-        int u = tid - 64;
+        int u = tid - 128;
         int t2 = tau - 1;
-        int b = u >> 2, j = u & 3, colgw = w * 4 + j;
-        float4 G = ((const float4*)gl2)[u];
+        int b = u >> 3, jn = u & 7, colgw = w * 8 + jn;
+        float gi = gl2[b * 33 + 0 * 8 + jn];
+        float gg = gl2[b * 33 + 1 * 8 + jn];
+        float gf = gl2[b * 33 + 2 * 8 + jn];
+        float go = gl2[b * 33 + 3 * 8 + jn];
         float cold = (tau == 1) ? 0.0f : cst2[u];
         float hold = (tau == 1) ? 0.0f : hst2[u];
-        float nc = sigm(G.z + 1.0f) * cold + sigm(G.x) * tanhf(G.y);
-        float nh = sigm(G.w) * tanhf(nc);
+        float nc = sigm(gf + 1.0f) * cold + sigm(gi) * tanhf(gg);
+        float nh = sigm(go) * tanhf(nc);
         size_t mi = ((size_t)b * 512 + t2) * 512 + colgw;
         bool mh = mask_at(zh2, mi, mmode);
         bool mc = mask_at(zc2, mi, mmode);
@@ -646,7 +738,7 @@
     vm0();
     __syncthreads();
     if (tid == 0)
-      __hip_atomic_fetch_add(cnt1 + (size_t)tau * 128 + (w >> 4) * 16, 1u,
+      __hip_atomic_fetch_add(cnt1 + (size_t)tau * 128 + (w >> 3) * 16, 1u,
                              __ATOMIC_RELAXED, __HIP_MEMORY_SCOPE_AGENT);
   }
 }
@@ -692,12 +784,13 @@
                MID = A_(4096 * 4), R5 = A_(16777216), R6 = A_(16777216), R7 = A_(25165824),
                D1X = A_(33554432), D2X = A_(33554432), MELP = A_(2621440);
   const size_t XA = R1, XB = R1 + 4194304;
-  const size_t XCOL3 = R2, ECWT = R3;
+  const size_t ECWT = R3;
   const size_t GF = R2;
   const size_t GB = R3, H1N = R3;
   const size_t ENC = R4, H2N = R4;
   const size_t COND = R5, PA = R5;
   const size_t PREA = R6, PREB = R6 + 8388608, PB = R6;
+  const size_t PBB = R3;
   const size_t DECIN = R7, RESID = R7;
   const size_t H1CB = R1, H1NB = R1 + 8388608;
   const size_t H2CB = R2;
@@ -706,8 +799,7 @@
   const size_t WT1 = R4, WT2 = R4 + 4194304;
   const size_t PROJA = R1;
   const size_t PRWT = R6;
-  const size_t XCOL80 = R1, W0T = R2;
-  const size_t XCOL = R1;
+  const size_t MELPB = R1, W0T = R2;
   const size_t WTP = D1X, W4T = D2X;
 
   auto F = [&](size_t off) { return (float*)(ws + off); };
@@ -731,23 +823,21 @@
   for (int i = 0; i < (int)(sizeof(cvs) / sizeof(cvs[0])); ++i)
     k_cvt<<<(cvs[i].n + 255) / 256, 256, 0, stream>>>(d_in[cvs[i].idx], F(cvs[i].off), cvs[i].n, flags);
 
-  k_embed<<<4096, 256, 0, stream>>>((const int*)d_in[0], F(C_EMB), F(XA));
+  k_embed<<<4096, 256, 0, stream>>>((const int*)d_in[0], F(C_EMB), F(XA), U(XAB));
   for (int i = 0; i < 3; ++i) {
-    k_i2c3<<<4096, 256, 0, stream>>>(F(XA), U(XCOL3));
     k_trbp<<<dim3(12, 4), 256, 0, stream>>>(F(C_ECW) + (size_t)i * 196608, 256, U(ECWT), 768, 768, 256, 256);
-    k_mf<0><<<dim3(64, 4), 256, 0, stream>>>(U(XCOL3), U(ECWT), nullptr, (void*)(ws + XB), 4096, 256, 768, 256);
+    k_mfc<3, 256, 256, 0><<<dim3(64, 4), 256, 0, stream>>>(U(XAB), U(ECWT), nullptr, (void*)(ws + XB), 4096, 256, 768, 256);
     k_cs1<<<256, 256, 0, stream>>>(F(XB), 16, 256, F(PARTS));
     k_cs2<<<256, 256, 0, stream>>>(F(PARTS), 256, 4096, F(STATS));
-    k_bnact<0><<<4096, 256, 0, stream>>>(F(XB), F(XA), F(STATS), F(C_EBS) + i * 256, F(C_EBO) + i * 256, 255, 1048576);
-  }
-  k_cvtb<<<4096, 256, 0, stream>>>(F(XA), U(XAB), 1048576);
+    k_bnact<0><<<4096, 256, 0, stream>>>(F(XB), F(XA), U(XAB), F(STATS), F(C_EBS) + i * 256, F(C_EBO) + i * 256, 255, 1048576);
+  }
   k_trbp<<<dim3(4, 16), 256, 0, stream>>>(F(C_LFW), 1024, U(WTE1), 256, 256, 1024, 1024);
   k_trbp<<<dim3(4, 16), 256, 0, stream>>>(F(C_LBW), 1024, U(WTE2), 256, 256, 1024, 1024);
   k_mf<3><<<dim3(64, 16), 256, 0, stream>>>(U(XAB), U(WTE1), F(C_LFB), (void*)(ws + GF), 4096, 1024, 256, 1024);
   k_mf<3><<<dim3(64, 16), 256, 0, stream>>>(U(XAB), U(WTE2), F(C_LBB), (void*)(ws + GB), 4096, 1024, 256, 1024);
   k_cumsum<<<1, 64, 0, stream>>>(F(C_DUR), F(MID));
-  k_enc_lstm<<<128, 256, 0, stream>>>(F(GF), F(GB), F(C_LFW), F(C_LBW), F(ENC), U(ENCB),
-                                      (const int*)d_in[1], cntE);
+  k_enc_lstm<<<64, 256, 0, stream>>>(F(GF), F(GB), F(C_LFW), F(C_LBW), F(ENC), U(ENCB),
+                                     (const int*)d_in[1], cntE);
   k_upsample<<<512, 256, 0, stream>>>(F(MID), F(ENC), F(COND));
 
   k_cvtbp<<<8192, 128, 0, stream>>>(F(C_MELS), U(MELB), 80, 96);
@@ -755,43 +845,41 @@
   k_mf<0><<<dim3(128, 4), 256, 0, stream>>>(U(MELB), U(PW1T), nullptr, (void*)(ws + PREA), 8192, 256, 96, 256);
   k_cs1<<<256, 256, 0, stream>>>(F(PREA), 32, 256, F(PARTS));
   k_cs2<<<256, 256, 0, stream>>>(F(PARTS), 256, 8192, F(STATS));
-  k_bnact<0><<<8192, 256, 0, stream>>>(F(PREA), F(PREB), F(STATS), F(C_P1S), F(C_P1O), 255, 2097152);
+  k_bnact<0><<<8192, 256, 0, stream>>>(F(PREA), F(PREB), nullptr, F(STATS), F(C_P1S), F(C_P1O), 255, 2097152);
   k_cvtb<<<8192, 256, 0, stream>>>(F(PREB), U(PREBB), 2097152);
   k_trbp<<<dim3(4, 4), 256, 0, stream>>>(F(C_PW2), 256, U(PW2T), 256, 256, 256, 256);
   k_mf<0><<<dim3(128, 4), 256, 0, stream>>>(U(PREBB), U(PW2T), nullptr, (void*)(ws + PREA), 8192, 256, 256, 256);
   k_cs1<<<256, 256, 0, stream>>>(F(PREA), 32, 256, F(PARTS));
   k_cs2<<<256, 256, 0, stream>>>(F(PARTS), 256, 8192, F(STATS));
-  k_bnact<0><<<8192, 256, 0, stream>>>(F(PREA), F(PREB), F(STATS), F(C_P2S), F(C_P2O), 255, 2097152);
+  k_bnact<0><<<8192, 256, 0, stream>>>(F(PREA), F(PREB), nullptr, F(STATS), F(C_P2S), F(C_P2O), 255, 2097152);
 
   k_concat<<<24576, 256, 0, stream>>>(F(COND), F(PREB), U(DECIN));
   k_trbp<<<dim3(12, 32), 256, 0, stream>>>(F(C_DW1), 2048, U(WT1), 768, 768, 2048, 2048);
   k_trbp<<<dim3(12, 32), 256, 0, stream>>>(F(C_DW2), 2048, U(WT2), 768, 768, 2048, 2048);
   k_mf<2><<<dim3(128, 32), 256, 0, stream>>>(U(DECIN), U(WT1), F(C_DB1), (void*)(ws + D1X), 8192, 2048, 768, 2048);
   k_mf<2><<<dim3(128, 32), 256, 0, stream>>>(U(DECIN), U(WT2), F(C_DB2), (void*)(ws + D2X), 8192, 2048, 768, 2048);
-  k_dec_lstm<<<128, 256, 0, stream>>>((const unsigned short*)(ws + D1X), (const unsigned short*)(ws + D2X),
-                                      F(C_DW1), F(C_DW2), d_in[4], d_in[5], d_in[6], d_in[7],
-                                      U(H1CB), U(H1NB), U(H2CB),
-                                      F(H1N), F(H2N), cnt1, flags);
+  k_dec_lstm<<<64, 256, 0, stream>>>((const unsigned short*)(ws + D1X), (const unsigned short*)(ws + D2X),
+                                     F(C_DW1), F(C_DW2), d_in[4], d_in[5], d_in[6], d_in[7],
+                                     U(H1CB), U(H1NB), U(H2CB),
+                                     F(H1N), F(H2N), cnt1, flags);
   k_cat3b<<<8192, 256, 0, stream>>>(F(COND), F(H1N), F(H2N), U(PROJA));
   k_trbp<<<dim3(24, 2), 256, 0, stream>>>(F(C_PRW), 80, U(PRWT), 1536, 1536, 80, 128);
   k_mf<4><<<dim3(128, 2), 256, 0, stream>>>(U(PROJA), U(PRWT), F(C_PRB), (void*)(ws + MELP), 8192, 128, 1536, 80);
 
-  k_i2c80<<<8192, 256, 0, stream>>>(F(MELP), U(XCOL80));
+  k_cvtb<<<2560, 256, 0, stream>>>(F(MELP), U(MELPB), 655360);
   k_trbp<<<dim3(7, 8), 256, 0, stream>>>(F(C_W0), 512, U(W0T), 400, 416, 512, 512);
-  k_mf<0><<<dim3(128, 8), 256, 0, stream>>>(U(XCOL80), U(W0T), nullptr, (void*)(ws + PA), 8192, 512, 416, 512);
+  k_mfc<5, 80, 512, 0><<<dim3(128, 8), 256, 0, stream>>>(U(MELPB), U(W0T), nullptr, (void*)(ws + PA), 8192, 512, 416, 512);
   k_cs1<<<256, 256, 0, stream>>>(F(PA), 32, 512, F(PARTS));
   k_cs2<<<512, 256, 0, stream>>>(F(PARTS), 512, 8192, F(STATS));
-  k_bnact<1><<<16384, 256, 0, stream>>>(F(PA), F(PB), F(STATS), F(C_PBS), F(C_PBO), 511, 4194304);
+  k_bnact<1><<<16384, 256, 0, stream>>>(F(PA), F(PB), U(PBB), F(STATS), F(C_PBS), F(C_PBO), 511, 4194304);
   for (int i = 0; i < 3; ++i) {
-    k_i2c<<<8192, 256, 0, stream>>>(F(PB), U(XCOL));
     k_trbp<<<dim3(40, 8), 256, 0, stream>>>(F(C_WM) + (size_t)i * 1310720, 512, U(WTP), 2560, 2560, 512, 512);
-    k_mf<0><<<dim3(128, 8), 256, 0, stream>>>(U(XCOL), U(WTP), nullptr, (void*)(ws + PA), 8192, 512, 2560, 512);
+    k_mfc<5, 512, 512, 0><<<dim3(128, 8), 256, 0, stream>>>(U(PBB), U(WTP), nullptr, (void*)(ws + PA), 8192, 512, 2560, 512);
     k_cs1<<<256, 256, 0, stream>>>(F(PA), 32, 512, F(PARTS));
     k_cs2<<<512, 256, 0, stream>>>(F(PARTS), 512, 8192, F(STATS));
-    k_bnact<1><<<16384, 256, 0, stream>>>(F(PA), F(PB), F(STATS), F(C_PBS) + (i + 1) * 512, F(C_PBO) + (i + 1) * 512, 511, 4194304);
-  }
-  k_i2c<<<8192, 256, 0, stream>>>(F(PB), U(XCOL));
+    k_bnact<1><<<16384, 256, 0, stream>>>(F(PA), F(PB), U(PBB), F(STATS), F(C_PBS) + (i + 1) * 512, F(C_PBO) + (i + 1) * 512, 511, 4194304);
+  }
   k_trbp<<<dim3(40, 2), 256, 0, stream>>>(F(C_W4), 80, U(W4T), 2560, 2560, 80, 128);
-  k_mf<4><<<dim3(128, 2), 256, 0, stream>>>(U(XCOL), U(W4T), F(C_B4), (void*)(ws + RESID), 8192, 128, 2560, 80);
+  k_mfc<5, 512, 512, 4><<<dim3(128, 2), 256, 0, stream>>>(U(PBB), U(W4T), F(C_B4), (void*)(ws + RESID), 8192, 128, 2560, 80);
   k_out<<<2560, 256, 0, stream>>>(F(MELP), F(RESID), d_out, flags);
 }
```
